# Optimization experiments

Hardware: AMD Instinct MI355X
Metric: run time of the kernel (lower is better)

Reference implementation:

```python
import jax, jax.numpy as jnp
import numpy as np

NUM_LEAVES = 8192
N_LAMBDA = 2101  # wavelengths 400..2500 nm

# ---- exponential integral E1(x), x > 0 (Abramowitz & Stegun 5.1.53 / 5.1.56) ----
# Ei(-x) = -E1(x) for x > 0; forward only ever calls expi on -kall with kall >= 1e-4.
_A = jnp.array([-0.57721566, 0.99999193, -0.24991055, 0.05519968, -0.00976004, 0.00107857], dtype=jnp.float32)
_PN = jnp.array([1.0, 8.5733287401, 18.0590169730, 8.6347608925, 0.2677737343], dtype=jnp.float32)
_PD = jnp.array([1.0, 9.5733223454, 25.6329561486, 21.0996530827, 3.9584969228], dtype=jnp.float32)

def _poly(c, x):
    r = c[0]
    for ci in c[1:]:
        r = r * x + ci
    return r

def _e1(x):
    # x > 0 guaranteed (kall clamped to >= 1e-4)
    small = -jnp.log(x) + _poly(_A[::-1], x)          # 0 < x <= 1
    big = jnp.exp(-x) / x * (_poly(_PN, x) / _poly(_PD, x))  # x > 1
    return jnp.where(x <= 1.0, small, big)

# ---- transmissivity of a dielectric plane (Stern / Allen) ----
def _getav(alpha_deg, nr):
    n2 = nr ** 2
    npx = n2 + 1.0
    nm = n2 - 1.0
    a = (nr + 1.0) * (nr + 1.0) / 2.0
    k = -(n2 - 1.0) * (n2 - 1.0) / 4.0
    rd = alpha_deg * (np.pi / 180.0)
    sa2 = np.sin(rd) ** 2  # python scalar
    if alpha_deg != 90.0:
        b1 = jnp.sqrt((sa2 - npx / 2.0) ** 2 + k)
    else:
        b1 = 0.0
    b2 = sa2 - npx / 2.0
    b = b1 - b2
    k2 = k ** 2
    ts = k2 / (6.0 * b ** 3) + k / b - b / 2.0 - (k2 / (6.0 * a ** 3) + k / a - a / 2.0)
    tp1 = -2.0 * n2 * (b - a) / npx ** 2
    nm2 = nm ** 2
    tp2 = -2.0 * n2 * npx * jnp.log(b / a) / nm2
    tp3 = n2 * (1.0 / b - 1.0 / a) / 2.0
    n22 = n2 ** 2
    npx3 = npx ** 3
    npax_a = 2.0 * npx * a - nm2
    npx_b = 2.0 * npx * b - nm2
    tp4 = 16.0 * n22 * (n22 + 1.0) * jnp.log(npx_b / npax_a) / (npx3 * nm2)
    tp5 = 16.0 * n2 ** 3 * (1.0 / npx_b - 1.0 / npax_a) / npx3
    tp = tp1 + tp2 + tp3 + tp4 + tp5
    return (ts + tp) / (2.0 * sa2)

def _forward(N, cab, car, water, lma, cant, nr, kab, kcar, kant, kw, km):
    # kall: [L, W] via broadcasting of [L,1] traits against [W] spectra
    kall = (cab * kab + car * kcar + cant * kant + water * kw + lma * km) / N
    kall = jnp.maximum(kall, 1e-4)
    # tau = (1-k)e^{-k} + k^2 * (-Ei(-k)) = (1-k)e^{-k} + k^2 E1(k)
    tau = (1.0 - kall) * jnp.exp(-kall) + kall ** 2 * _e1(kall)

    # one-layer reflectance/transmittance
    talf = _getav(40.0, nr)
    ralf = 1.0 - talf
    t12 = _getav(90.0, nr)
    r12 = 1.0 - t12
    t21 = t12 / (nr * nr)
    r21 = 1.0 - t21
    denom = 1.0 - r21 * r21 * tau * tau
    Ta = talf * tau * t21 / denom
    Ra = ralf + r21 * tau * Ta
    t = t12 * tau * t21 / denom
    r = r12 + r21 * tau * t

    rpt = r + t
    rmt = r - t
    mask = rpt >= 1.0  # [L, W]
    Dsq = (1.0 + rpt) * (1.0 + rmt) * (1.0 - rmt) * (1.0 - rpt)
    D = jnp.sqrt(jnp.where(mask, 1.0, Dsq))
    rqmtq = r ** 2 - t ** 2
    a = (1.0 + rqmtq + D) / (2.0 * r)
    b = (1.0 - rqmtq + D) / (2.0 * t)
    b_safe = jnp.where(mask, 1.0, b)  # guard pow with float exponent
    bnm1 = b_safe ** (N - 1.0)
    bn2 = bnm1 ** 2
    a2 = a * a
    den2 = a2 * bn2 - 1.0
    Rsub = a * (bn2 - 1.0) / den2
    Tsub = bnm1 * (a2 - 1.0) / den2
    # thick-layer (r+t >= 1) limit
    Tsub_alt = t / (t + (1.0 - t) * (N - 1.0))
    Tsub = jnp.where(mask, Tsub_alt, Tsub)
    Rsub = jnp.where(mask, 1.0 - Tsub_alt, Rsub)

    den3 = 1.0 - Rsub * r
    tran = Ta * Tsub / den3
    refl = Ra + Ta_Rsub_term(Ta, Rsub, t, den3)
    return refl, tran

def Ta_Rsub_term(Ta, Rsub, t, den3):
    return Ta * Rsub * t / den3

def setup_inputs() -> dict:
    key = jax.random.key(0)
    ks = jax.random.split(key, 12)
    u = lambda k, shp: jax.random.uniform(k, shp, dtype=jnp.float32)
    L, W = NUM_LEAVES, N_LAMBDA
    return {
        "N":     1.0 + 1.5 * u(ks[0], (L, 1)),      # leaf structure 1..2.5
        "cab":   10.0 + 70.0 * u(ks[1], (L, 1)),    # chlorophyll ug/cm2
        "car":   2.0 + 18.0 * u(ks[2], (L, 1)),     # carotenoids
        "water": 0.002 + 0.03 * u(ks[3], (L, 1)),   # EWT cm
        "lma":   0.005 + 0.03 * u(ks[4], (L, 1)),   # dry matter g/cm2
        "cant":  2.0 * u(ks[5], (L, 1)),            # anthocyanins
        "nr":    1.3 + 0.3 * u(ks[6], (W,)),        # refractive index
        "kab":   0.05 * u(ks[7], (W,)),
        "kcar":  0.05 * u(ks[8], (W,)),
        "kant":  0.05 * u(ks[9], (W,)),
        "kw":    30.0 * u(ks[10], (W,)),
        "km":    60.0 * u(ks[11], (W,)),
    }

def reference(N, cab, car, water, lma, cant, nr, kab, kcar, kant, kw, km):
    return _forward(N, cab, car, water, lma, cant, nr, kab, kcar, kant, kw, km)
```

## Files before the change

### kernel.cpp

```cpp
#include <hip/hip_runtime.h>

#define L_LEAVES 8192
#define W_LAMBDA 2101
#define WPAD     2104
#define SA2_40   0.41317591116653485f
#define LOG2E_F  1.4426950408889634f
#define LN2_F    0.6931471805599453f

__device__ __forceinline__ float rcpf(float x)  { return __builtin_amdgcn_rcpf(x); }
__device__ __forceinline__ float log2f_fast(float x) { return __builtin_amdgcn_logf(x); }
__device__ __forceinline__ float exp2f_fast(float x) { return __builtin_amdgcn_exp2f(x); }
__device__ __forceinline__ float sqrtf_fast(float x) { return __builtin_amdgcn_sqrtf(x); }

__device__ __forceinline__ float getav_dev(float sa2, bool is90, float nr) {
    float n2  = nr * nr;
    float npx = n2 + 1.0f;
    float nm  = n2 - 1.0f;
    float a   = (nr + 1.0f) * (nr + 1.0f) * 0.5f;
    float k   = -(n2 - 1.0f) * (n2 - 1.0f) * 0.25f;
    float b2  = sa2 - npx * 0.5f;
    float b1  = is90 ? 0.0f : sqrtf(b2 * b2 + k);
    float b   = b1 - b2;
    float k2  = k * k;
    float b3  = b * b * b;
    float a3  = a * a * a;
    float ts  = k2 / (6.0f * b3) + k / b - b * 0.5f
              - (k2 / (6.0f * a3) + k / a - a * 0.5f);
    float tp1 = -2.0f * n2 * (b - a) / (npx * npx);
    float nm2 = nm * nm;
    float tp2 = -2.0f * n2 * npx * logf(b / a) / nm2;
    float tp3 = n2 * (1.0f / b - 1.0f / a) * 0.5f;
    float n22 = n2 * n2;
    float npx3 = npx * npx * npx;
    float npax_a = 2.0f * npx * a - nm2;
    float npx_b  = 2.0f * npx * b - nm2;
    float tp4 = 16.0f * n22 * (n22 + 1.0f) * logf(npx_b / npax_a) / (npx3 * nm2);
    float tp5 = 16.0f * n2 * n2 * n2 * (1.0f / npx_b - 1.0f / npax_a) / npx3;
    float tp  = tp1 + tp2 + tp3 + tp4 + tp5;
    return (ts + tp) / (2.0f * sa2);
}

__global__ void precompute_kernel(const float* __restrict__ nr, float* __restrict__ tab) {
    int w = blockIdx.x * blockDim.x + threadIdx.x;
    if (w >= W_LAMBDA) return;
    float n    = nr[w];
    float talf = getav_dev(SA2_40, false, n);
    float t12  = getav_dev(1.0f,   true,  n);
    float t21  = t12 * rcpf(n * n);
    float r21  = 1.0f - t21;
    tab[0 * WPAD + w] = talf * t21;
    tab[1 * WPAD + w] = 1.0f - talf;
    tab[2 * WPAD + w] = t12 * t21;
    tab[3 * WPAD + w] = 1.0f - t12;
    tab[4 * WPAD + w] = r21;
    tab[5 * WPAD + w] = r21 * r21;
}

struct f4u { float v[4]; };

__device__ __forceinline__ float vget(const float4& v, int j) {
    return j == 0 ? v.x : (j == 1 ? v.y : (j == 2 ? v.z : v.w));
}

template<bool USE_TAB>
__global__ __launch_bounds__(192) void prospect_kernel(
    const float* __restrict__ pN,   const float* __restrict__ pcab,
    const float* __restrict__ pcar, const float* __restrict__ pwater,
    const float* __restrict__ plma, const float* __restrict__ pcant,
    const float* __restrict__ pnr,
    const float* __restrict__ pkab, const float* __restrict__ pkcar,
    const float* __restrict__ pkant, const float* __restrict__ pkw,
    const float* __restrict__ pkm,
    const float* __restrict__ tab,
    float* __restrict__ out)
{
    const int q  = blockIdx.x * blockDim.x + threadIdx.x;
    const int w0 = q * 4;
    if (w0 >= W_LAMBDA) return;
    const bool full = (w0 + 4 <= W_LAMBDA);

    const int l = blockIdx.y;
    const float Nl   = pN[l];
    const float invN = rcpf(Nl);
    const float Nm1  = Nl - 1.0f;
    const float cabl = pcab[l], carl = pcar[l], cantl = pcant[l];
    const float watl = pwater[l], lmal = plma[l];
    const size_t LW = (size_t)L_LEAVES * W_LAMBDA;

    float4 vkab, vkcar, vkant, vkw, vkm;
    float4 t0, t1, t2, t3, t4, t5;
    if (full) {
        vkab  = *(const float4*)(pkab  + w0);
        vkcar = *(const float4*)(pkcar + w0);
        vkant = *(const float4*)(pkant + w0);
        vkw   = *(const float4*)(pkw   + w0);
        vkm   = *(const float4*)(pkm   + w0);
    } else {
        #pragma unroll
        for (int j = 0; j < 4; ++j) {
            int w = min(w0 + j, W_LAMBDA - 1);
            ((float*)&vkab)[j]  = pkab[w];
            ((float*)&vkcar)[j] = pkcar[w];
            ((float*)&vkant)[j] = pkant[w];
            ((float*)&vkw)[j]   = pkw[w];
            ((float*)&vkm)[j]   = pkm[w];
        }
    }
    if (USE_TAB) {
        if (full) {
            t0 = *(const float4*)(tab + 0 * WPAD + w0);
            t1 = *(const float4*)(tab + 1 * WPAD + w0);
            t2 = *(const float4*)(tab + 2 * WPAD + w0);
            t3 = *(const float4*)(tab + 3 * WPAD + w0);
            t4 = *(const float4*)(tab + 4 * WPAD + w0);
            t5 = *(const float4*)(tab + 5 * WPAD + w0);
        } else {
            #pragma unroll
            for (int j = 0; j < 4; ++j) {
                int w = min(w0 + j, W_LAMBDA - 1);
                ((float*)&t0)[j] = tab[0 * WPAD + w];
                ((float*)&t1)[j] = tab[1 * WPAD + w];
                ((float*)&t2)[j] = tab[2 * WPAD + w];
                ((float*)&t3)[j] = tab[3 * WPAD + w];
                ((float*)&t4)[j] = tab[4 * WPAD + w];
                ((float*)&t5)[j] = tab[5 * WPAD + w];
            }
        }
    } else {
        #pragma unroll
        for (int j = 0; j < 4; ++j) {
            int w = min(w0 + j, W_LAMBDA - 1);
            float n    = pnr[w];
            float talf = getav_dev(SA2_40, false, n);
            float t12  = getav_dev(1.0f,   true,  n);
            float t21  = t12 * rcpf(n * n);
            float r21  = 1.0f - t21;
            ((float*)&t0)[j] = talf * t21;
            ((float*)&t1)[j] = 1.0f - talf;
            ((float*)&t2)[j] = t12 * t21;
            ((float*)&t3)[j] = 1.0f - t12;
            ((float*)&t4)[j] = r21;
            ((float*)&t5)[j] = r21 * r21;
        }
    }

    float rf[4], tr[4];
    #pragma unroll
    for (int j = 0; j < 4; ++j) {
        const float c0 = vget(t0, j), c1 = vget(t1, j), c2 = vget(t2, j);
        const float c3 = vget(t3, j), c4 = vget(t4, j), c5 = vget(t5, j);

        float k = (cabl * vget(vkab, j) + carl * vget(vkcar, j) + cantl * vget(vkant, j)
                 + watl * vget(vkw, j) + lmal * vget(vkm, j)) * invN;
        k = fmaxf(k, 1e-4f);

        float ek   = exp2f_fast(-k * LOG2E_F);
        float lg2k = log2f_fast(k);
        float poly = fmaf(fmaf(fmaf(fmaf(fmaf(0.00107857f, k, -0.00976004f), k, 0.05519968f),
                        k, -0.24991055f), k, 0.99999193f), k, -0.57721566f);
        float e1s  = fmaf(-LN2_F, lg2k, poly);
        float taus = fmaf(k * k, e1s, fmaf(-k, ek, ek));
        float pn = fmaf(fmaf(fmaf(k + 8.5733287401f, k, 18.0590169730f),
                       k, 8.6347608925f), k, 0.2677737343f);
        float pd = fmaf(fmaf(fmaf(k + 9.5733223454f, k, 25.6329561486f),
                       k, 21.0996530827f), k, 3.9584969228f);
        float taub = ek * fmaf(k, pn - pd, pd) * rcpf(pd);
        float tau  = (k <= 1.0f) ? taus : taub;

        float tau2 = tau * tau;
        float rd   = rcpf(fmaf(-c5, tau2, 1.0f));
        float trd  = tau * rd;
        float Ta   = c0 * trd;
        float tt   = c2 * trd;
        float r21t = c4 * tau;
        float Ra   = fmaf(r21t, Ta, c1);
        float rr   = fmaf(r21t, tt, c3);

        float rpt  = rr + tt;
        float rmt  = rr - tt;
        bool  mask = (rpt >= 1.0f);
        float Dsq  = fmaf(-rmt, rmt, 1.0f) * fmaf(-rpt, rpt, 1.0f);
        float D    = sqrtf_fast(mask ? 1.0f : Dsq);
        float rq   = rpt * rmt;
        float s1   = 1.0f + D;
        float rp2  = rcpf((rr * tt) * 4.0f);
        float aa   = (s1 + rq) * (rp2 * (tt + tt));
        float bb   = (s1 - rq) * (rp2 * (rr + rr));
        float bsafe = mask ? 1.0f : bb;
        float bnm1 = exp2f_fast(Nm1 * log2f_fast(bsafe));
        float bn2  = bnm1 * bnm1;
        float a2   = aa * aa;
        float den2 = fmaf(a2, bn2, -1.0f);
        float bn2m1 = bn2 - 1.0f;
        float aarr  = aa * rr;
        float M     = fmaf(-aarr, bn2m1, den2);
        float invM  = rcpf(M);
        float TaM   = Ta * invM;
        float tranj = TaM * bnm1 * (a2 - 1.0f);
        float reflj = fmaf(TaM * tt * aa, bn2m1, Ra);

        if (__any((int)mask)) {
            float Talt = tt * rcpf(fmaf(Nm1, 1.0f - tt, tt));
            float Rsm  = 1.0f - Talt;
            float g    = Ta * rcpf(fmaf(-Rsm, rr, 1.0f));
            if (mask) { tranj = g * Talt; reflj = fmaf(g * Rsm, tt, Ra); }
        }

        tr[j] = tranj;
        rf[j] = reflj;
    }

    const size_t base = (size_t)l * W_LAMBDA + w0;
    if (full) {
        f4u fr; f4u ft;
        #pragma unroll
        for (int j = 0; j < 4; ++j) { fr.v[j] = rf[j]; ft.v[j] = tr[j]; }
        *reinterpret_cast<f4u*>(out + base)      = fr;
        *reinterpret_cast<f4u*>(out + LW + base) = ft;
    } else {
        out[base]      = rf[0];
        out[LW + base] = tr[0];
    }
}

extern "C" void kernel_launch(void* const* d_in, const int* in_sizes, int n_in,
                              void* d_out, int out_size, void* d_ws, size_t ws_size,
                              hipStream_t stream) {
    const float* pN     = (const float*)d_in[0];
    const float* pcab   = (const float*)d_in[1];
    const float* pcar   = (const float*)d_in[2];
    const float* pwater = (const float*)d_in[3];
    const float* plma   = (const float*)d_in[4];
    const float* pcant  = (const float*)d_in[5];
    const float* pnr    = (const float*)d_in[6];
    const float* pkab   = (const float*)d_in[7];
    const float* pkcar  = (const float*)d_in[8];
    const float* pkant  = (const float*)d_in[9];
    const float* pkw    = (const float*)d_in[10];
    const float* pkm    = (const float*)d_in[11];
    float* out = (float*)d_out;

    const int nquads = (W_LAMBDA + 3) / 4;
    dim3 grid((nquads + 191) / 192, L_LEAVES);
    dim3 block(192);

    const size_t tab_bytes = 6 * WPAD * sizeof(float);
    if (ws_size >= tab_bytes) {
        float* tabp = (float*)d_ws;
        precompute_kernel<<<(W_LAMBDA + 255) / 256, 256, 0, stream>>>(pnr, tabp);
        prospect_kernel<true><<<grid, block, 0, stream>>>(
            pN, pcab, pcar, pwater, plma, pcant, pnr,
            pkab, pkcar, pkant, pkw, pkm, (const float*)tabp, out);
    } else {
        prospect_kernel<false><<<grid, block, 0, stream>>>(
            pN, pcab, pcar, pwater, plma, pcant, pnr,
            pkab, pkcar, pkant, pkw, pkm, nullptr, out);
    }
}
```

Measured before the change: 60.03 us.

## Flatten grid to a 1D leaf-by-quad mapping and drop the r21-squared table

Replaces the 2D grid (three 192-thread blocks per leaf, with idle tail lanes) with a 1D grid of 256-thread blocks that exactly covers all leaf×quad pairs. Each thread's leaf and wavelength offset now come from a division, which removes the idle threads that padded each leaf row. It also drops the sixth precomputed table row and recomputes r21·tau squared inline, which removes the tail-guarded table load path. Output indexing moves to 32-bit offsets with separate reflectance and transmittance pointers. The cost is an integer divide per thread and loads of uninitialised table padding for the last quad, whose values are not used.

```diff
diff --git a/kernel.cpp b/kernel.cpp
--- a/kernel.cpp
+++ b/kernel.cpp
@@ -2,6 +2,7 @@
 
 #define L_LEAVES 8192
 #define W_LAMBDA 2101
+#define QPL      526
 #define WPAD     2104
 #define SA2_40   0.41317591116653485f
 #define LOG2E_F  1.4426950408889634f
@@ -53,7 +54,6 @@
     tab[2 * WPAD + w] = t12 * t21;
     tab[3 * WPAD + w] = 1.0f - t12;
     tab[4 * WPAD + w] = r21;
-    tab[5 * WPAD + w] = r21 * r21;
 }
 
 struct f4u { float v[4]; };
@@ -63,7 +63,7 @@
 }
 
 template<bool USE_TAB>
-__global__ __launch_bounds__(192) void prospect_kernel(
+__global__ __launch_bounds__(256) void prospect_kernel(
     const float* __restrict__ pN,   const float* __restrict__ pcab,
     const float* __restrict__ pcar, const float* __restrict__ pwater,
     const float* __restrict__ plma, const float* __restrict__ pcant,
@@ -72,23 +72,21 @@
     const float* __restrict__ pkant, const float* __restrict__ pkw,
     const float* __restrict__ pkm,
     const float* __restrict__ tab,
-    float* __restrict__ out)
+    float* __restrict__ out_r, float* __restrict__ out_t)
 {
-    const int q  = blockIdx.x * blockDim.x + threadIdx.x;
-    const int w0 = q * 4;
-    if (w0 >= W_LAMBDA) return;
+    const int q  = blockIdx.x * 256 + threadIdx.x;
+    const int l  = q / QPL;
+    const int w0 = (q - l * QPL) * 4;
     const bool full = (w0 + 4 <= W_LAMBDA);
 
-    const int l = blockIdx.y;
     const float Nl   = pN[l];
     const float invN = rcpf(Nl);
     const float Nm1  = Nl - 1.0f;
     const float cabl = pcab[l], carl = pcar[l], cantl = pcant[l];
     const float watl = pwater[l], lmal = plma[l];
-    const size_t LW = (size_t)L_LEAVES * W_LAMBDA;
 
     float4 vkab, vkcar, vkant, vkw, vkm;
-    float4 t0, t1, t2, t3, t4, t5;
+    float4 t0, t1, t2, t3, t4;
     if (full) {
         vkab  = *(const float4*)(pkab  + w0);
         vkcar = *(const float4*)(pkcar + w0);
@@ -107,25 +105,11 @@
         }
     }
     if (USE_TAB) {
-        if (full) {
-            t0 = *(const float4*)(tab + 0 * WPAD + w0);
-            t1 = *(const float4*)(tab + 1 * WPAD + w0);
-            t2 = *(const float4*)(tab + 2 * WPAD + w0);
-            t3 = *(const float4*)(tab + 3 * WPAD + w0);
-            t4 = *(const float4*)(tab + 4 * WPAD + w0);
-            t5 = *(const float4*)(tab + 5 * WPAD + w0);
-        } else {
-            #pragma unroll
-            for (int j = 0; j < 4; ++j) {
-                int w = min(w0 + j, W_LAMBDA - 1);
-                ((float*)&t0)[j] = tab[0 * WPAD + w];
-                ((float*)&t1)[j] = tab[1 * WPAD + w];
-                ((float*)&t2)[j] = tab[2 * WPAD + w];
-                ((float*)&t3)[j] = tab[3 * WPAD + w];
-                ((float*)&t4)[j] = tab[4 * WPAD + w];
-                ((float*)&t5)[j] = tab[5 * WPAD + w];
-            }
-        }
+        t0 = *(const float4*)(tab + 0 * WPAD + w0);
+        t1 = *(const float4*)(tab + 1 * WPAD + w0);
+        t2 = *(const float4*)(tab + 2 * WPAD + w0);
+        t3 = *(const float4*)(tab + 3 * WPAD + w0);
+        t4 = *(const float4*)(tab + 4 * WPAD + w0);
     } else {
         #pragma unroll
         for (int j = 0; j < 4; ++j) {
@@ -140,7 +124,6 @@
             ((float*)&t2)[j] = t12 * t21;
             ((float*)&t3)[j] = 1.0f - t12;
             ((float*)&t4)[j] = r21;
-            ((float*)&t5)[j] = r21 * r21;
         }
     }
 
@@ -148,7 +131,7 @@
     #pragma unroll
     for (int j = 0; j < 4; ++j) {
         const float c0 = vget(t0, j), c1 = vget(t1, j), c2 = vget(t2, j);
-        const float c3 = vget(t3, j), c4 = vget(t4, j), c5 = vget(t5, j);
+        const float c3 = vget(t3, j), c4 = vget(t4, j);
 
         float k = (cabl * vget(vkab, j) + carl * vget(vkcar, j) + cantl * vget(vkant, j)
                  + watl * vget(vkw, j) + lmal * vget(vkm, j)) * invN;
@@ -167,12 +150,11 @@
         float taub = ek * fmaf(k, pn - pd, pd) * rcpf(pd);
         float tau  = (k <= 1.0f) ? taus : taub;
 
-        float tau2 = tau * tau;
-        float rd   = rcpf(fmaf(-c5, tau2, 1.0f));
+        float r21t = c4 * tau;
+        float rd   = rcpf(fmaf(-r21t, r21t, 1.0f));
         float trd  = tau * rd;
         float Ta   = c0 * trd;
         float tt   = c2 * trd;
-        float r21t = c4 * tau;
         float Ra   = fmaf(r21t, Ta, c1);
         float rr   = fmaf(r21t, tt, c3);
 
@@ -192,10 +174,9 @@
         float a2   = aa * aa;
         float den2 = fmaf(a2, bn2, -1.0f);
         float bn2m1 = bn2 - 1.0f;
-        float aarr  = aa * rr;
-        float M     = fmaf(-aarr, bn2m1, den2);
-        float invM  = rcpf(M);
-        float TaM   = Ta * invM;
+        float M    = fmaf(-aa * rr, bn2m1, den2);
+        float invM = rcpf(M);
+        float TaM  = Ta * invM;
         float tranj = TaM * bnm1 * (a2 - 1.0f);
         float reflj = fmaf(TaM * tt * aa, bn2m1, Ra);
 
@@ -210,16 +191,16 @@
         rf[j] = reflj;
     }
 
-    const size_t base = (size_t)l * W_LAMBDA + w0;
+    const unsigned base = (unsigned)l * W_LAMBDA + (unsigned)w0;
     if (full) {
         f4u fr; f4u ft;
         #pragma unroll
         for (int j = 0; j < 4; ++j) { fr.v[j] = rf[j]; ft.v[j] = tr[j]; }
-        *reinterpret_cast<f4u*>(out + base)      = fr;
-        *reinterpret_cast<f4u*>(out + LW + base) = ft;
-    } else {
-        out[base]      = rf[0];
-        out[LW + base] = tr[0];
+        *reinterpret_cast<f4u*>(out_r + base) = fr;
+        *reinterpret_cast<f4u*>(out_t + base) = ft;
+    } else {
+        out_r[base] = rf[0];
+        out_t[base] = tr[0];
     }
 }
 
@@ -238,22 +219,23 @@
     const float* pkant  = (const float*)d_in[9];
     const float* pkw    = (const float*)d_in[10];
     const float* pkm    = (const float*)d_in[11];
-    float* out = (float*)d_out;
-
-    const int nquads = (W_LAMBDA + 3) / 4;
-    dim3 grid((nquads + 191) / 192, L_LEAVES);
-    dim3 block(192);
-
-    const size_t tab_bytes = 6 * WPAD * sizeof(float);
+    float* out_r = (float*)d_out;
+    float* out_t = out_r + (size_t)L_LEAVES * W_LAMBDA;
+
+    const int nquads = L_LEAVES * QPL;
+    dim3 grid(nquads / 256);
+    dim3 block(256);
+
+    const size_t tab_bytes = 5 * WPAD * sizeof(float);
     if (ws_size >= tab_bytes) {
         float* tabp = (float*)d_ws;
         precompute_kernel<<<(W_LAMBDA + 255) / 256, 256, 0, stream>>>(pnr, tabp);
         prospect_kernel<true><<<grid, block, 0, stream>>>(
             pN, pcab, pcar, pwater, plma, pcant, pnr,
-            pkab, pkcar, pkant, pkw, pkm, (const float*)tabp, out);
+            pkab, pkcar, pkant, pkw, pkm, (const float*)tabp, out_r, out_t);
     } else {
         prospect_kernel<false><<<grid, block, 0, stream>>>(
             pN, pcab, pcar, pwater, plma, pcant, pnr,
-            pkab, pkcar, pkant, pkw, pkm, nullptr, out);
-    }
-}
+            pkab, pkcar, pkant, pkw, pkm, nullptr, out_r, out_t);
+    }
+}
```

Measured after the change: 104.3 us. +73.8%, slower.
